# Kernel optimization log

Measured on AMD Instinct MI355X. Metric: run time of the kernel, lower is better.

The kernel has to match this reference:

```python
import jax, jax.numpy as jnp
import numpy as np

N_HEADS = 16
N_KV_HEADS = 4
HEAD_DIM = 64
ROPE_BASE = 10000.0

def _rope_cos_sin(T, dtype):
    # flash-attn style: cos/sin of shape [T, head_dim//2]
    inv_freq = 1.0 / (ROPE_BASE ** (jnp.arange(0, HEAD_DIM, 2, dtype=jnp.float32) / HEAD_DIM))
    freqs = jnp.arange(T, dtype=jnp.float32)[:, None] * inv_freq[None, :]  # [T, D/2]
    return jnp.cos(freqs).astype(dtype), jnp.sin(freqs).astype(dtype)

def _apply_rope(x, cos, sin):
    # x: [B, H, T, D], non-interleaved rotate-half on full head dim
    d2 = HEAD_DIM // 2
    x1, x2 = x[..., :d2], x[..., d2:]
    c = cos[None, None, :, :]
    s = sin[None, None, :, :]
    return jnp.concatenate([x1 * c - x2 * s, x2 * c + x1 * s], axis=-1)

def setup_inputs() -> dict:
    key = jax.random.key(0)
    ks = jax.random.split(key, 6)
    B, T, D = 1, 4096, 1024
    def g(k, shape, scale):
        return jax.random.normal(k, shape, dtype=jnp.float32) * scale
    return {
        "query": g(ks[0], (B, T, D), 1.0),
        "Wq": g(ks[1], (D, D), D ** -0.5),
        "Wk": g(ks[2], (D, N_KV_HEADS * HEAD_DIM), D ** -0.5),
        "Wv": g(ks[3], (D, N_KV_HEADS * HEAD_DIM), D ** -0.5),
        "W1": g(ks[4], (D, 4 * D), D ** -0.5),
        "W2": g(ks[5], (4 * D, D), (4 * D) ** -0.5),
    }

def reference(query, Wq, Wk, Wv, W1, W2):
    B, T, D = query.shape
    # QKV projections -> [B, H, T, Dh]
    q = (query @ Wq).reshape(B, T, N_HEADS, HEAD_DIM).transpose(0, 2, 1, 3)
    k = (query @ Wk).reshape(B, T, N_KV_HEADS, HEAD_DIM).transpose(0, 2, 1, 3)
    v = (query @ Wv).reshape(B, T, N_KV_HEADS, HEAD_DIM).transpose(0, 2, 1, 3)
    # RoPE (seqlen_offset = 0, no cache)
    cos, sin = _rope_cos_sin(T, q.dtype)
    q = _apply_rope(q, cos, sin)
    k = _apply_rope(k, cos, sin)
    # GQA: repeat KV heads to match Q heads
    n_rep = N_HEADS // N_KV_HEADS
    k = jnp.repeat(k, n_rep, axis=1)
    v = jnp.repeat(v, n_rep, axis=1)
    # Scaled dot-product attention, causal
    scale = HEAD_DIM ** -0.5
    scores = jnp.einsum("bhqd,bhkd->bhqk", q, k) * scale
    i = jnp.arange(T)[:, None]
    j = jnp.arange(T)[None, :]
    scores = jnp.where(j > i, jnp.finfo(scores.dtype).min, scores)
    attn = jax.nn.softmax(scores, axis=-1)
    out = jnp.einsum("bhqk,bhkd->bhqd", attn, v)  # [B, H, T, Dh]
    out = out.transpose(0, 2, 1, 3).reshape(B, T, D)
    # out_proj: Linear -> SiLU -> Linear (use_swiglu=True path)
    return jax.nn.silu(out @ W1) @ W2
```

## Files before the change

### kernel.cpp

```cpp
#include <hip/hip_runtime.h>
#include <stdint.h>

typedef unsigned short u16;
typedef __bf16 bf16x8 __attribute__((ext_vector_type(8)));
typedef float f32x4 __attribute__((ext_vector_type(4)));

#define T_SEQ 4096
#define DMODEL 1024

__device__ __forceinline__ float bf2f(u16 x) {
  union { uint32_t u; float f; } v; v.u = ((uint32_t)x) << 16; return v.f;
}
__device__ __forceinline__ u16 f2bf(float f) {
  union { float f; uint32_t u; } v; v.f = f;
  return (u16)((v.u + 0x7FFFu + ((v.u >> 16) & 1u)) >> 16);
}
__device__ __forceinline__ float fexp2(float x) {
#if __has_builtin(__builtin_amdgcn_exp2f)
  return __builtin_amdgcn_exp2f(x);
#else
  return __expf(x * 0.6931471805599453f);
#endif
}
__device__ __forceinline__ uint32_t pack_bf16(float lo, float hi) {
#if __has_builtin(__builtin_amdgcn_cvt_pk_bf16_f32)
  typedef __bf16 bf16x2_t __attribute__((ext_vector_type(2)));
  union { bf16x2_t v; uint32_t u; } c;
  c.v = __builtin_amdgcn_cvt_pk_bf16_f32(lo, hi);
  return c.u;
#else
  union { float f; uint32_t u; } a, b;
  a.f = lo; b.f = hi;
  return __builtin_amdgcn_perm(b.u + 0x8000u, a.u + 0x8000u, 0x07060302u);
#endif
}
__device__ __forceinline__ void async16(void* lds, const void* g) {
  __builtin_amdgcn_global_load_lds(
      (__attribute__((address_space(1))) void*)const_cast<void*>(g),
      (__attribute__((address_space(3))) void*)lds, 16, 0, 0);
}
__device__ __forceinline__ void storeC(u16* C, size_t i, float v) { C[i] = f2bf(v); }
__device__ __forceinline__ void storeC(float* C, size_t i, float v) { C[i] = v; }

__device__ __forceinline__ void wtrans_body(const float* __restrict__ in,
                                            u16* __restrict__ out, int K, int N,
                                            int bx, int by, int tid,
                                            float (*tile)[65]) {
  const int n0 = bx * 64, k0 = by * 64;
  const int r = tid >> 2, c = (tid & 3) * 16;
#pragma unroll
  for (int j = 0; j < 4; ++j) {
    float4 v = *(const float4*)&in[(size_t)(k0 + r) * N + n0 + c + j * 4];
    tile[r][c + j * 4 + 0] = v.x; tile[r][c + j * 4 + 1] = v.y;
    tile[r][c + j * 4 + 2] = v.z; tile[r][c + j * 4 + 3] = v.w;
  }
  __syncthreads();
  union { u16 s[16]; uint4 q[2]; } buf;
#pragma unroll
  for (int j = 0; j < 16; ++j) buf.s[j] = f2bf(tile[c + j][r]);
  u16* dst = out + (size_t)(n0 + r) * K + k0 + c;
  *(uint4*)(dst) = buf.q[0];
  *(uint4*)(dst + 8) = buf.q[1];
}

__global__ void __launch_bounds__(256) prep(const float* __restrict__ query,
                                            const float* __restrict__ Wq,
                                            const float* __restrict__ Wk,
                                            const float* __restrict__ Wv,
                                            const float* __restrict__ W1,
                                            const float* __restrict__ W2,
                                            u16* __restrict__ Xb,
                                            u16* __restrict__ WqkvT,
                                            u16* __restrict__ W1T,
                                            u16* __restrict__ W2T) {
  __shared__ float tile[64][65];
  const int b = blockIdx.x, tid = threadIdx.x;
  if (b < 4096) {
    int idx = (b * 256 + tid) * 4;
    float4 v = *(const float4*)(query + idx);
    union { u16 s[4]; uint2 q; } o;
    o.s[0] = f2bf(v.x); o.s[1] = f2bf(v.y); o.s[2] = f2bf(v.z); o.s[3] = f2bf(v.w);
    *(uint2*)(Xb + idx) = o.q;
  } else if (b < 4352) {
    int t = b - 4096;
    wtrans_body(Wq, WqkvT, 1024, 1024, t & 15, t >> 4, tid, tile);
  } else if (b < 4416) {
    int t = b - 4352;
    wtrans_body(Wk, WqkvT + (size_t)1024 * 1024, 1024, 256, t & 3, t >> 2, tid, tile);
  } else if (b < 4480) {
    int t = b - 4416;
    wtrans_body(Wv, WqkvT + (size_t)1280 * 1024, 1024, 256, t & 3, t >> 2, tid, tile);
  } else if (b < 5504) {
    int t = b - 4480;
    wtrans_body(W1, W1T, 1024, 4096, t & 63, t >> 6, tid, tile);
  } else {
    int t = b - 5504;
    wtrans_body(W2, W2T, 4096, 1024, t & 15, t >> 4, tid, tile);
  }
}

__global__ void __launch_bounds__(256) rope_vt(const u16* __restrict__ qkv,
                                               u16* __restrict__ Q,
                                               u16* __restrict__ Ko,
                                               u16* __restrict__ Vt) {
  __shared__ u16 tile[64][65];
  const int b = blockIdx.x, tid = threadIdx.x;
  if (b < 4096) {
    const int t = b;
    const int i = tid & 31;
    const float ang = (float)t * powf(10000.f, -(float)i * (1.f / 32.f));
    float s, c;
    sincosf(ang, &s, &c);
    const u16* row = qkv + (size_t)t * 1536;
    const float QS = 0.125f * 1.4426950408889634f;
    const float cq = c * QS, sq = s * QS;
#pragma unroll
    for (int it = 0; it < 2; ++it) {
      int h = (tid >> 5) + it * 8;
      float x1 = bf2f(row[h * 64 + i]);
      float x2 = bf2f(row[h * 64 + 32 + i]);
      size_t o = ((size_t)h * T_SEQ + t) * 64 + i;
      Q[o] = f2bf(x1 * cq - x2 * sq);
      Q[o + 32] = f2bf(x2 * cq + x1 * sq);
    }
    if (tid < 128) {
      int h = tid >> 5;
      float x1 = bf2f(row[1024 + h * 64 + i]);
      float x2 = bf2f(row[1024 + h * 64 + 32 + i]);
      size_t o = ((size_t)h * T_SEQ + t) * 64 + i;
      Ko[o] = f2bf(x1 * c - x2 * s);
      Ko[o + 32] = f2bf(x2 * c + x1 * s);
    }
  } else {
    const int t = b - 4096;
    const int t0 = (t & 63) * 64, h = t >> 6;
    const int r = tid >> 2, q4 = (tid & 3) * 16;
    const u16* src = qkv + (size_t)(t0 + r) * 1536 + 1280 + h * 64 + q4;
    union { u16 s[16]; uint4 q[2]; } buf;
    buf.q[0] = *(const uint4*)(src);
    buf.q[1] = *(const uint4*)(src + 8);
#pragma unroll
    for (int j = 0; j < 16; ++j) tile[r][q4 + j] = buf.s[j];
    __syncthreads();
#pragma unroll
    for (int j = 0; j < 16; ++j) buf.s[j] = tile[q4 + j][r];
    u16* dst = Vt + ((size_t)h * 64 + r) * T_SEQ + t0 + q4;
    *(uint4*)(dst) = buf.q[0];
    *(uint4*)(dst + 8) = buf.q[1];
  }
}

template <int AM, int ACT, typename OutT>
__global__ void __launch_bounds__(256) gemm_bt(const u16* __restrict__ A,
                                               const u16* __restrict__ Bt,
                                               OutT* __restrict__ C,
                                               int M, int N, int K) {
  __shared__ u16 sA[AM * 32][64];
  __shared__ u16 sB[128][64];
  const int tid = threadIdx.x;
  const int w = tid >> 6, lane = tid & 63;
  const int g = lane >> 4, l15 = lane & 15;
  const int r8 = lane >> 3, c8 = lane & 7;
  const int bm = blockIdx.y * (AM * 32), bn = blockIdx.x * 128;

  f32x4 acc[AM][4];
#pragma unroll
  for (int i = 0; i < AM; ++i)
#pragma unroll
    for (int j = 0; j < 4; ++j) acc[i][j] = (f32x4){0.f, 0.f, 0.f, 0.f};

  const u16* Ag = A + (size_t)(bm + w * (AM * 8) + r8) * K + (c8 ^ r8) * 8;
  const u16* Bg = Bt + (size_t)(bn + w * 32 + r8) * K + (c8 ^ r8) * 8;
  const int mrow = (w >> 1) * (AM * 16), ncol = (w & 1) * 64;
  const int swz = l15 & 7;

  for (int k0 = 0; k0 < K; k0 += 64) {
#pragma unroll
    for (int t = 0; t < AM; ++t)
      async16(&sA[w * (AM * 8) + t * 8][0], Ag + (size_t)(t * 8) * K + k0);
#pragma unroll
    for (int t = 0; t < 4; ++t)
      async16(&sB[w * 32 + t * 8][0], Bg + (size_t)(t * 8) * K + k0);
    __syncthreads();
#pragma unroll
    for (int kk = 0; kk < 2; ++kk) {
      const int cb = ((kk * 4 + g) ^ swz) * 8;
      bf16x8 a[AM], b[4];
#pragma unroll
      for (int i = 0; i < AM; ++i) a[i] = *(const bf16x8*)&sA[mrow + i * 16 + l15][cb];
#pragma unroll
      for (int i = 0; i < 4; ++i) b[i] = *(const bf16x8*)&sB[ncol + i * 16 + l15][cb];
#pragma unroll
      for (int mi = 0; mi < AM; ++mi)
#pragma unroll
        for (int ni = 0; ni < 4; ++ni)
          acc[mi][ni] = __builtin_amdgcn_mfma_f32_16x16x32_bf16(a[mi], b[ni], acc[mi][ni], 0, 0, 0);
    }
    __syncthreads();
  }
#pragma unroll
  for (int mi = 0; mi < AM; ++mi)
#pragma unroll
    for (int ni = 0; ni < 4; ++ni)
#pragma unroll
      for (int r = 0; r < 4; ++r) {
        int row = bm + mrow + mi * 16 + g * 4 + r;
        int col = bn + ncol + ni * 16 + l15;
        float v = acc[mi][ni][r];
        if (ACT == 1) v = v / (1.f + __expf(-v));
        storeC(C, (size_t)row * N + col, v);
      }
}

__global__ void __launch_bounds__(256, 2) gemm_w2(const u16* __restrict__ A,
                                                  const u16* __restrict__ Bt,
                                                  float* __restrict__ C0,
                                                  u16* __restrict__ C1) {
  __shared__ u16 sA[128][64];
  __shared__ u16 sB[128][64];
  const int K = 4096, N = 1024;
  const int z = blockIdx.z, koff = z * 2048;
  const int tid = threadIdx.x;
  const int w = tid >> 6, lane = tid & 63;
  const int g = lane >> 4, l15 = lane & 15;
  const int r8 = lane >> 3, c8 = lane & 7;
  const int bm = blockIdx.y * 128, bn = blockIdx.x * 128;

  f32x4 acc[4][4];
#pragma unroll
  for (int i = 0; i < 4; ++i)
#pragma unroll
    for (int j = 0; j < 4; ++j) acc[i][j] = (f32x4){0.f, 0.f, 0.f, 0.f};

  const u16* Ag = A + (size_t)(bm + w * 32 + r8) * K + koff + (c8 ^ r8) * 8;
  const u16* Bg = Bt + (size_t)(bn + w * 32 + r8) * K + koff + (c8 ^ r8) * 8;
  const int mrow = (w >> 1) * 64, ncol = (w & 1) * 64;
  const int swz = l15 & 7;

  for (int k0 = 0; k0 < 2048; k0 += 64) {
#pragma unroll
    for (int t = 0; t < 4; ++t) {
      async16(&sA[w * 32 + t * 8][0], Ag + (size_t)(t * 8) * K + k0);
      async16(&sB[w * 32 + t * 8][0], Bg + (size_t)(t * 8) * K + k0);
    }
    __syncthreads();
#pragma unroll
    for (int kk = 0; kk < 2; ++kk) {
      const int cb = ((kk * 4 + g) ^ swz) * 8;
      bf16x8 a[4], b[4];
#pragma unroll
      for (int i = 0; i < 4; ++i) {
        a[i] = *(const bf16x8*)&sA[mrow + i * 16 + l15][cb];
        b[i] = *(const bf16x8*)&sB[ncol + i * 16 + l15][cb];
      }
#pragma unroll
      for (int mi = 0; mi < 4; ++mi)
#pragma unroll
        for (int ni = 0; ni < 4; ++ni)
          acc[mi][ni] = __builtin_amdgcn_mfma_f32_16x16x32_bf16(a[mi], b[ni], acc[mi][ni], 0, 0, 0);
    }
    __syncthreads();
  }
#pragma unroll
  for (int mi = 0; mi < 4; ++mi)
#pragma unroll
    for (int ni = 0; ni < 4; ++ni)
#pragma unroll
      for (int r = 0; r < 4; ++r) {
        size_t idx = (size_t)(bm + mrow + mi * 16 + g * 4 + r) * N + bn + ncol + ni * 16 + l15;
        if (z == 0) C0[idx] = acc[mi][ni][r];
        else        C1[idx] = f2bf(acc[mi][ni][r]);
      }
}

__global__ void __launch_bounds__(256) w2_combine(float* __restrict__ out,
                                                  const u16* __restrict__ P1) {
  int idx = (blockIdx.x * 256 + threadIdx.x) * 4;
  float4 v = *(const float4*)(out + idx);
  union { uint2 q; u16 s[4]; } p;
  p.q = *(const uint2*)(P1 + idx);
  v.x += bf2f(p.s[0]); v.y += bf2f(p.s[1]);
  v.z += bf2f(p.s[2]); v.w += bf2f(p.s[3]);
  *(float4*)(out + idx) = v;
}

__global__ void __launch_bounds__(256, 2) attn(const u16* __restrict__ Q,
                                               const u16* __restrict__ K,
                                               const u16* __restrict__ Vt,
                                               u16* __restrict__ O0,
                                               u16* __restrict__ O1,
                                               float* __restrict__ L0,
                                               float* __restrict__ L1) {
  __shared__ u16 sK[2][64][64];
  __shared__ u16 sV[2][64][64];
  __shared__ u16 sP[4][64][68];
  const int pr = blockIdx.x >> 1;
  const int split = blockIdx.x & 1;
  const int h = blockIdx.y;
  const int kvh = h >> 2;
  const int tid = threadIdx.x;
  const int w = tid >> 6, lane = tid & 63;
  const int g = lane >> 4, l15 = lane & 15;
  const int r8 = lane >> 3, c8 = lane & 7;
  const int swz = l15 & 7;
  const int t0 = pr, t1 = 31 - pr;
  const int off = split * 64;

  u16* Op = split ? O1 : O0;
  float* Lp = split ? L1 : L0;

  bf16x8 qf[2][2][2];
  {
    const u16* Qh = Q + (size_t)h * T_SEQ * 64;
#pragma unroll
    for (int half = 0; half < 2; ++half)
#pragma unroll
      for (int mi = 0; mi < 2; ++mi) {
        const int q = (half ? t1 : t0) * 128 + w * 32 + mi * 16 + l15;
#pragma unroll
        for (int kk = 0; kk < 2; ++kk)
          qf[half][mi][kk] = *(const bf16x8*)(Qh + (size_t)q * 64 + (kk * 4 + g) * 8);
      }
  }

  f32x4 oacc[2][2][4];
  f32x4 lacc[2][2];
#pragma unroll
  for (int half = 0; half < 2; ++half)
#pragma unroll
    for (int mi = 0; mi < 2; ++mi) {
      lacc[half][mi] = (f32x4){0.f, 0.f, 0.f, 0.f};
#pragma unroll
      for (int nd = 0; nd < 4; ++nd) oacc[half][mi][nd] = (f32x4){0.f, 0.f, 0.f, 0.f};
    }

  bf16x8 ONES;
  {
    union { u16 s[8]; bf16x8 v; } o;
#pragma unroll
    for (int i = 0; i < 8; ++i) o.s[i] = 0x3F80;
    ONES = o.v;
  }

  const u16* Kg = K + ((size_t)kvh * T_SEQ + w * 16 + r8) * 64 + (c8 ^ r8) * 8;
  const u16* Vg = Vt + ((size_t)kvh * 64 + w * 16 + r8) * T_SEQ + (c8 ^ r8) * 8;

#define STAGE(J, B)                                                     \
  {                                                                     \
    const int kv0_ = (J) * 64;                                          \
    async16(&sK[B][w * 16 + 0][0], Kg + (size_t)kv0_ * 64);             \
    async16(&sK[B][w * 16 + 8][0], Kg + (size_t)(kv0_ + 8) * 64);       \
    async16(&sV[B][w * 16 + 0][0], Vg + kv0_);                          \
    async16(&sV[B][w * 16 + 8][0], Vg + (size_t)8 * T_SEQ + kv0_);      \
  }

#define BODY(B, ACT0, M0, M1)                                                     \
  {                                                                               \
    const int b_ = (B);                                                           \
    f32x4 s1[2][4], s0[2][4];                                                     \
    _Pragma("unroll") for (int mi = 0; mi < 2; ++mi)                              \
    _Pragma("unroll") for (int kt = 0; kt < 4; ++kt) {                            \
      s1[mi][kt] = (f32x4){0.f, 0.f, 0.f, 0.f};                                   \
      if (ACT0) s0[mi][kt] = (f32x4){0.f, 0.f, 0.f, 0.f};                         \
    }                                                                             \
    __builtin_amdgcn_s_setprio(1);                                                \
    _Pragma("unroll") for (int kt = 0; kt < 4; ++kt)                              \
    _Pragma("unroll") for (int kk = 0; kk < 2; ++kk) {                            \
      bf16x8 kf = *(const bf16x8*)&sK[b_][kt * 16 + l15][((kk * 4 + g) ^ swz) * 8]; \
      _Pragma("unroll") for (int mi = 0; mi < 2; ++mi) {                          \
        s1[mi][kt] = __builtin_amdgcn_mfma_f32_16x16x32_bf16(kf, qf[1][mi][kk], s1[mi][kt], 0, 0, 0); \
        if (ACT0)                                                                 \
          s0[mi][kt] = __builtin_amdgcn_mfma_f32_16x16x32_bf16(kf, qf[0][mi][kk], s0[mi][kt], 0, 0, 0); \
      }                                                                           \
    }                                                                             \
    __builtin_amdgcn_s_setprio(0);                                                \
    _Pragma("unroll") for (int mi = 0; mi < 2; ++mi) {                            \
      const int thr_ = w * 32 + mi * 16 + l15 - off;                              \
      _Pragma("unroll") for (int kt = 0; kt < 4; ++kt) {                          \
        float p_[4];                                                              \
        _Pragma("unroll") for (int r = 0; r < 4; ++r) {                           \
          float p = fexp2(s1[mi][kt][r]);                                         \
          if (M1 && (kt * 16 + g * 4 + r > thr_)) p = 0.f;                        \
          p_[r] = p;                                                              \
        }                                                                         \
        uint2 pk;                                                                 \
        pk.x = pack_bf16(p_[0], p_[1]);                                           \
        pk.y = pack_bf16(p_[2], p_[3]);                                           \
        *(uint2*)&sP[w][32 + mi * 16 + l15][kt * 16 + g * 4] = pk;                \
      }                                                                           \
      if (ACT0) {                                                                 \
        _Pragma("unroll") for (int kt = 0; kt < 4; ++kt) {                        \
          float p_[4];                                                            \
          _Pragma("unroll") for (int r = 0; r < 4; ++r) {                         \
            float p = fexp2(s0[mi][kt][r]);                                       \
            if (M0 && (kt * 16 + g * 4 + r > thr_)) p = 0.f;                      \
            p_[r] = p;                                                            \
          }                                                                       \
          uint2 pk;                                                               \
          pk.x = pack_bf16(p_[0], p_[1]);                                         \
          pk.y = pack_bf16(p_[2], p_[3]);                                         \
          *(uint2*)&sP[w][mi * 16 + l15][kt * 16 + g * 4] = pk;                   \
        }                                                                         \
      }                                                                           \
    }                                                                             \
    __builtin_amdgcn_wave_barrier();          \
    __builtin_amdgcn_s_setprio(1);                                                \
    _Pragma("unroll") for (int kk = 0; kk < 2; ++kk) {                            \
      bf16x8 pf1[2], pf0[2];                                                      \
      _Pragma("unroll") for (int mi = 0; mi < 2; ++mi) {                          \
        pf1[mi] = *(const bf16x8*)&sP[w][32 + mi * 16 + l15][kk * 32 + g * 8];    \
        if (ACT0) pf0[mi] = *(const bf16x8*)&sP[w][mi * 16 + l15][kk * 32 + g * 8]; \
      }                                                                           \
      _Pragma("unroll") for (int mi = 0; mi < 2; ++mi) {                          \
        lacc[1][mi] = __builtin_amdgcn_mfma_f32_16x16x32_bf16(pf1[mi], ONES, lacc[1][mi], 0, 0, 0); \
        if (ACT0)                                                                 \
          lacc[0][mi] = __builtin_amdgcn_mfma_f32_16x16x32_bf16(pf0[mi], ONES, lacc[0][mi], 0, 0, 0); \
      }                                                                           \
      _Pragma("unroll") for (int nd = 0; nd < 4; ++nd) {                          \
        bf16x8 vf = *(const bf16x8*)&sV[b_][nd * 16 + l15][((kk * 4 + g) ^ swz) * 8]; \
        _Pragma("unroll") for (int mi = 0; mi < 2; ++mi) {                        \
          oacc[1][mi][nd] = __builtin_amdgcn_mfma_f32_16x16x32_bf16(pf1[mi], vf, oacc[1][mi][nd], 0, 0, 0); \
          if (ACT0)                                                               \
            oacc[0][mi][nd] = __builtin_amdgcn_mfma_f32_16x16x32_bf16(pf0[mi], vf, oacc[0][mi][nd], 0, 0, 0); \
        }                                                                         \
      }                                                                           \
    }                                                                             \
    __builtin_amdgcn_s_setprio(0);                                                \
  }

  const int e0 = 2 * t0 + split, e1 = 2 * t1 + split;
  STAGE(split, 0);
  int jj = split, b = 0;
  for (; jj < e0; jj += 2, b ^= 1) {
    __syncthreads();
    STAGE(jj + 2, b ^ 1);
    BODY(b, true, false, false);
  }
  {
    __syncthreads();
    STAGE(jj + 2, b ^ 1);
    BODY(b, true, true, false);
    jj += 2; b ^= 1;
  }
  for (; jj < e1; jj += 2, b ^= 1) {
    __syncthreads();
    STAGE(jj + 2, b ^ 1);
    BODY(b, false, false, false);
  }
  {
    __syncthreads();
    BODY(b, false, false, true);
  }
#undef STAGE
#undef BODY

#pragma unroll
  for (int half = 0; half < 2; ++half) {
    const int tb = (half ? t1 : t0) * 128;
#pragma unroll
    for (int mi = 0; mi < 2; ++mi)
#pragma unroll
      for (int r = 0; r < 4; ++r) {
        const int trow = tb + w * 32 + mi * 16 + g * 4 + r;
#pragma unroll
        for (int nd = 0; nd < 4; ++nd)
          Op[(size_t)trow * DMODEL + h * 64 + nd * 16 + l15] = f2bf(oacc[half][mi][nd][r]);
        if (l15 == 0) Lp[h * T_SEQ + trow] = lacc[half][mi][r];
      }
  }
}

__global__ void __launch_bounds__(256) attn_combine(const u16* __restrict__ O0,
                                                    const u16* __restrict__ O1,
                                                    const float* __restrict__ L0,
                                                    const float* __restrict__ L1,
                                                    u16* __restrict__ AO) {
  const int t = blockIdx.x, tid = threadIdx.x;
  const int h = tid >> 4, d4 = (tid & 15) * 4;
  const float inv = 1.f / (L0[h * T_SEQ + t] + L1[h * T_SEQ + t]);
  const size_t idx = (size_t)t * DMODEL + h * 64 + d4;
  union { uint2 q; u16 s[4]; } a, b, o;
  a.q = *(const uint2*)(O0 + idx);
  b.q = *(const uint2*)(O1 + idx);
#pragma unroll
  for (int i = 0; i < 4; ++i) o.s[i] = f2bf((bf2f(a.s[i]) + bf2f(b.s[i])) * inv);
  *(uint2*)(AO + idx) = o.q;
}

extern "C" void kernel_launch(void* const* d_in, const int* in_sizes, int n_in,
                              void* d_out, int out_size, void* d_ws, size_t ws_size,
                              hipStream_t stream) {
  const float* query = (const float*)d_in[0];
  const float* Wq = (const float*)d_in[1];
  const float* Wk = (const float*)d_in[2];
  const float* Wv = (const float*)d_in[3];
  const float* W1 = (const float*)d_in[4];
  const float* W2 = (const float*)d_in[5];
  float* out = (float*)d_out;

  char* ws = (char*)d_ws;
  size_t off = 0;
  auto alloc = [&](size_t bytes) { char* p = ws + off; off += (bytes + 255) & ~(size_t)255; return p; };
  u16* Xb   = (u16*)alloc((size_t)4096 * 1024 * 2);
  u16* QKVb = (u16*)alloc((size_t)4096 * 1536 * 2);
  u16* Qb   = (u16*)alloc((size_t)16 * 4096 * 64 * 2);
  u16* Kb   = (u16*)alloc((size_t)4 * 4096 * 64 * 2);
  u16* Vtb  = (u16*)alloc((size_t)4 * 4096 * 64 * 2);
  u16* H    = (u16*)ws;
  u16*   O0p = Xb;
  u16*   O1p = QKVb;
  float* L0p = (float*)(QKVb + (size_t)4096 * 1024);
  float* L1p = L0p + 16 * T_SEQ;
  u16* WqkvT = (u16*)alloc((size_t)1536 * 1024 * 2);
  u16* W1T   = (u16*)alloc((size_t)4096 * 1024 * 2);
  u16* W2T   = (u16*)alloc((size_t)1024 * 4096 * 2);
  u16* AO    = (u16*)alloc((size_t)4096 * 1024 * 2);
  u16* P1    = W1T;
  (void)ws_size; (void)in_sizes; (void)n_in; (void)out_size;

  prep<<<6528, 256, 0, stream>>>(query, Wq, Wk, Wv, W1, W2, Xb, WqkvT, W1T, W2T);
  gemm_bt<2, 0, u16><<<dim3(12, 64), 256, 0, stream>>>(Xb, WqkvT, QKVb, 4096, 1536, 1024);
  rope_vt<<<4352, 256, 0, stream>>>(QKVb, Qb, Kb, Vtb);
  attn<<<dim3(32, 16), 256, 0, stream>>>(Qb, Kb, Vtb, O0p, O1p, L0p, L1p);
  attn_combine<<<4096, 256, 0, stream>>>(O0p, O1p, L0p, L1p, AO);
  gemm_bt<4, 1, u16><<<dim3(32, 32), 256, 0, stream>>>(AO, W1T, H, 4096, 4096, 1024);
  gemm_w2<<<dim3(8, 32, 2), 256, 0, stream>>>(H, W2T, out, P1);
  w2_combine<<<4096, 256, 0, stream>>>(out, P1);
}
```

Measured before the change: 291.5 us.

## Double-buffer LDS tiles in the projection and W2 GEMM kernels

Both GEMM kernels now use two shared-memory stages. The next K tile's async global-to-LDS loads are issued right after the barrier, then the MFMA work runs on the current stage, so loads overlap compute and one barrier per iteration is removed. The cost is double the LDS footprint per block, which may lower occupancy. The extra vmcnt waits at the barrier may also limit how much overlap is actually achieved.

```diff
diff --git a/kernel.cpp b/kernel.cpp
--- a/kernel.cpp
+++ b/kernel.cpp
@@ -155,8 +155,8 @@
                                                const u16* __restrict__ Bt,
                                                OutT* __restrict__ C,
                                                int M, int N, int K) {
-  __shared__ u16 sA[AM * 32][64];
-  __shared__ u16 sB[128][64];
+  __shared__ u16 sA[2][AM * 32][64];
+  __shared__ u16 sB[2][128][64];
   const int tid = threadIdx.x;
   const int w = tid >> 6, lane = tid & 63;
   const int g = lane >> 4, l15 = lane & 15;
@@ -174,30 +174,36 @@
   const int mrow = (w >> 1) * (AM * 16), ncol = (w & 1) * 64;
   const int swz = l15 & 7;
 
+#define GSTAGE(K0, BUF)                                                        \
+  {                                                                            \
+    _Pragma("unroll") for (int t = 0; t < AM; ++t)                             \
+      async16(&sA[BUF][w * (AM * 8) + t * 8][0], Ag + (size_t)(t * 8) * K + (K0)); \
+    _Pragma("unroll") for (int t = 0; t < 4; ++t)                              \
+      async16(&sB[BUF][w * 32 + t * 8][0], Bg + (size_t)(t * 8) * K + (K0));   \
+  }
+
+  GSTAGE(0, 0);
+  int cur = 0;
   for (int k0 = 0; k0 < K; k0 += 64) {
-#pragma unroll
-    for (int t = 0; t < AM; ++t)
-      async16(&sA[w * (AM * 8) + t * 8][0], Ag + (size_t)(t * 8) * K + k0);
-#pragma unroll
-    for (int t = 0; t < 4; ++t)
-      async16(&sB[w * 32 + t * 8][0], Bg + (size_t)(t * 8) * K + k0);
-    __syncthreads();
+    __syncthreads();
+    if (k0 + 64 < K) GSTAGE(k0 + 64, cur ^ 1);
 #pragma unroll
     for (int kk = 0; kk < 2; ++kk) {
       const int cb = ((kk * 4 + g) ^ swz) * 8;
       bf16x8 a[AM], b[4];
 #pragma unroll
-      for (int i = 0; i < AM; ++i) a[i] = *(const bf16x8*)&sA[mrow + i * 16 + l15][cb];
-#pragma unroll
-      for (int i = 0; i < 4; ++i) b[i] = *(const bf16x8*)&sB[ncol + i * 16 + l15][cb];
+      for (int i = 0; i < AM; ++i) a[i] = *(const bf16x8*)&sA[cur][mrow + i * 16 + l15][cb];
+#pragma unroll
+      for (int i = 0; i < 4; ++i) b[i] = *(const bf16x8*)&sB[cur][ncol + i * 16 + l15][cb];
 #pragma unroll
       for (int mi = 0; mi < AM; ++mi)
 #pragma unroll
         for (int ni = 0; ni < 4; ++ni)
           acc[mi][ni] = __builtin_amdgcn_mfma_f32_16x16x32_bf16(a[mi], b[ni], acc[mi][ni], 0, 0, 0);
     }
-    __syncthreads();
-  }
+    cur ^= 1;
+  }
+#undef GSTAGE
 #pragma unroll
   for (int mi = 0; mi < AM; ++mi)
 #pragma unroll
@@ -216,8 +222,8 @@
                                                   const u16* __restrict__ Bt,
                                                   float* __restrict__ C0,
                                                   u16* __restrict__ C1) {
-  __shared__ u16 sA[128][64];
-  __shared__ u16 sB[128][64];
+  __shared__ u16 sA[2][128][64];
+  __shared__ u16 sB[2][128][64];
   const int K = 4096, N = 1024;
   const int z = blockIdx.z, koff = z * 2048;
   const int tid = threadIdx.x;
@@ -237,21 +243,27 @@
   const int mrow = (w >> 1) * 64, ncol = (w & 1) * 64;
   const int swz = l15 & 7;
 
+#define GSTAGE(K0, BUF)                                                   \
+  {                                                                       \
+    _Pragma("unroll") for (int t = 0; t < 4; ++t) {                       \
+      async16(&sA[BUF][w * 32 + t * 8][0], Ag + (size_t)(t * 8) * K + (K0)); \
+      async16(&sB[BUF][w * 32 + t * 8][0], Bg + (size_t)(t * 8) * K + (K0)); \
+    }                                                                     \
+  }
+
+  GSTAGE(0, 0);
+  int cur = 0;
   for (int k0 = 0; k0 < 2048; k0 += 64) {
-#pragma unroll
-    for (int t = 0; t < 4; ++t) {
-      async16(&sA[w * 32 + t * 8][0], Ag + (size_t)(t * 8) * K + k0);
-      async16(&sB[w * 32 + t * 8][0], Bg + (size_t)(t * 8) * K + k0);
-    }
-    __syncthreads();
+    __syncthreads();
+    if (k0 + 64 < 2048) GSTAGE(k0 + 64, cur ^ 1);
 #pragma unroll
     for (int kk = 0; kk < 2; ++kk) {
       const int cb = ((kk * 4 + g) ^ swz) * 8;
       bf16x8 a[4], b[4];
 #pragma unroll
       for (int i = 0; i < 4; ++i) {
-        a[i] = *(const bf16x8*)&sA[mrow + i * 16 + l15][cb];
-        b[i] = *(const bf16x8*)&sB[ncol + i * 16 + l15][cb];
+        a[i] = *(const bf16x8*)&sA[cur][mrow + i * 16 + l15][cb];
+        b[i] = *(const bf16x8*)&sB[cur][ncol + i * 16 + l15][cb];
       }
 #pragma unroll
       for (int mi = 0; mi < 4; ++mi)
@@ -259,8 +271,9 @@
         for (int ni = 0; ni < 4; ++ni)
           acc[mi][ni] = __builtin_amdgcn_mfma_f32_16x16x32_bf16(a[mi], b[ni], acc[mi][ni], 0, 0, 0);
     }
-    __syncthreads();
-  }
+    cur ^= 1;
+  }
+#undef GSTAGE
 #pragma unroll
   for (int mi = 0; mi < 4; ++mi)
 #pragma unroll
```

Measured after the change: 278.4 us. 4.5% less time.
